# Kernel optimization log

Hardware: AMD Instinct MI355X
Metric: run time of the kernel (lower is better)

The kernel has to match this reference:

```python
import jax, jax.numpy as jnp
import numpy as np

N = 50000        # nodes
E = 1600000      # edges (before self-loops)
HID = 128
HEADS = 4
HD = HID // HEADS
FIN = 32 + 7     # node feats + scenario feats
EPS = 1e-5


def _ln(x, g, b):
    m = x.mean(-1, keepdims=True)
    v = ((x - m) ** 2).mean(-1, keepdims=True)
    return (x - m) / jnp.sqrt(v + EPS) * g + b


def _gat(x, src, dst, W, a_s, a_d, bias):
    # PyG GATConv (concat=True, negative_slope=0.2), eval mode (no dropout)
    xp = (x @ W).reshape(-1, HEADS, HD)                    # [N,H,C]
    es = (xp * a_s).sum(-1)                                # [N,H]
    ed = (xp * a_d).sum(-1)                                # [N,H]
    e = jax.nn.leaky_relu(es[src] + ed[dst], 0.2)          # [Etot,H]
    emax = jax.ops.segment_max(e, dst, num_segments=N)     # per-target softmax (self-loops guarantee nonempty segments)
    a = jnp.exp(e - emax[dst])
    denom = jax.ops.segment_sum(a, dst, num_segments=N)
    a = a / denom[dst]
    out = jax.ops.segment_sum(xp[src] * a[:, :, None], dst, num_segments=N)
    return out.reshape(-1, HID) + bias


def setup_inputs() -> dict:
    key = jax.random.key(0)
    ks = iter(jax.random.split(key, 64))

    def rn(shape, scale=0.05):
        return jax.random.normal(next(ks), shape, dtype=jnp.float32) * scale

    inp = {}
    inp["x"] = jax.random.normal(next(ks), (N, FIN), dtype=jnp.float32)
    inp["edge_index"] = jax.random.randint(next(ks), (2, E), 0, N)
    inp["enc_w1"] = rn((FIN, HID)); inp["enc_b1"] = jnp.zeros((HID,), jnp.float32)
    inp["enc_w2"] = rn((HID, HID)); inp["enc_b2"] = jnp.zeros((HID,), jnp.float32)
    for l in (1, 2, 3):
        inp[f"W{l}"] = rn((HID, HID))
        inp[f"as{l}"] = rn((HEADS, HD))
        inp[f"ad{l}"] = rn((HEADS, HD))
        inp[f"bc{l}"] = jnp.zeros((HID,), jnp.float32)
        inp[f"g{l}"] = jnp.ones((HID,), jnp.float32)
        inp[f"be{l}"] = jnp.zeros((HID,), jnp.float32)
    inp["imp_w1"] = rn((HID, HID // 2)); inp["imp_b1"] = jnp.zeros((HID // 2,), jnp.float32)
    inp["imp_w2"] = rn((HID // 2, 3));   inp["imp_b2"] = jnp.zeros((3,), jnp.float32)
    inp["tim_w1"] = rn((HID, HID // 2)); inp["tim_b1"] = jnp.zeros((HID // 2,), jnp.float32)
    inp["tim_w2"] = rn((HID // 2, 2));   inp["tim_b2"] = jnp.zeros((2,), jnp.float32)
    return inp


def reference(x, edge_index, enc_w1, enc_b1, enc_w2, enc_b2,
              W1, as1, ad1, bc1, g1, be1,
              W2, as2, ad2, bc2, g2, be2,
              W3, as3, ad3, bc3, g3, be3,
              imp_w1, imp_b1, imp_w2, imp_b2,
              tim_w1, tim_b1, tim_w2, tim_b2):
    loops = jnp.arange(N, dtype=edge_index.dtype)          # add_self_loops=True
    src = jnp.concatenate([edge_index[0], loops])
    dst = jnp.concatenate([edge_index[1], loops])
    h = jax.nn.relu(x @ enc_w1 + enc_b1) @ enc_w2 + enc_b2
    for (W, a_s, a_d, bc, g, be) in ((W1, as1, ad1, bc1, g1, be1),
                                     (W2, as2, ad2, bc2, g2, be2),
                                     (W3, as3, ad3, bc3, g3, be3)):
        h = jax.nn.relu(_ln(_gat(h, src, dst, W, a_s, a_d, bc) + h, g, be))
    impact = jax.nn.relu(h @ imp_w1 + imp_b1) @ imp_w2 + imp_b2
    timing = jax.nn.softplus(jax.nn.relu(h @ tim_w1 + tim_b1) @ tim_w2 + tim_b2)
    return (impact, timing)
```

## Files before the change

kernel.cpp:

```cpp
#include <hip/hip_runtime.h>
#include <hip/hip_bf16.h>
#include <math.h>

#define NN 50000
#define EDGES 1600000
#define ETOT (EDGES + NN)
#define FINDIM 39
#define NPART 128
#define PSZ 391
#define PCAP 14000
#define P1TILE 4096

__device__ __forceinline__ unsigned pack_bf16(float a, float b) {
    __hip_bfloat162 t;
    t.x = __float2bfloat16(a);
    t.y = __float2bfloat16(b);
    return *(unsigned*)&t;
}
__device__ __forceinline__ float2 unpack_bf16(unsigned w) {
    float2 r;
    r.x = __uint_as_float(w << 16);
    r.y = __uint_as_float(w & 0xffff0000u);
    return r;
}

__device__ __forceinline__ int src_at(const int* ei, int i, bool i32) {
    return i32 ? ei[i] : ei[2 * i];
}
__device__ __forceinline__ int dst_at(const int* ei, int i, bool i32) {
    return i32 ? ei[EDGES + i] : ei[2 * (EDGES + i)];
}

__global__ __launch_bounds__(256) void pass1_kernel(const int* __restrict__ ei,
                                                    int* __restrict__ gcursor,
                                                    unsigned* __restrict__ pbuf) {
    __shared__ unsigned raw[P1TILE];
    __shared__ unsigned srt[P1TILE];
    __shared__ int pcnt[NPART], poff[NPART], pcur[NPART], gb[NPART];
    __shared__ int i32flag;
    int t = threadIdx.x;
    if (t == 0) i32flag = 0;
    __syncthreads();
    int chunk = (ETOT + gridDim.x - 1) / gridDim.x;
    int c0 = blockIdx.x * chunk;
    int c1 = c0 + chunk; if (c1 > ETOT) c1 = ETOT;
    int sb = c0 < EDGES - 64 ? c0 : 0;
    if (t < 64 && ei[2 * (sb + t) + 1] != 0) i32flag = 1;
    __syncthreads();
    bool i32 = (i32flag != 0);
    for (int t0 = c0; t0 < c1; t0 += P1TILE) {
        int tn = c1 - t0; if (tn > P1TILE) tn = P1TILE;
        if (t < NPART) { pcnt[t] = 0; pcur[t] = 0; }
        __syncthreads();
        for (int i = t; i < tn; i += 256) {
            int e = t0 + i;
            int s, d;
            if (e < EDGES) { s = src_at(ei, e, i32); d = dst_at(ei, e, i32); }
            else { s = d = e - EDGES; }
            raw[i] = ((unsigned)s << 16) | (unsigned)d;
            atomicAdd(&pcnt[d / PSZ], 1);
        }
        __syncthreads();
        if (t < NPART) poff[t] = pcnt[t];
        __syncthreads();
        for (int off = 1; off < NPART; off <<= 1) {
            int v = 0;
            if (t < NPART && t >= off) v = poff[t - off];
            __syncthreads();
            if (t < NPART) poff[t] += v;
            __syncthreads();
        }
        if (t < NPART) {
            poff[t] -= pcnt[t];
            gb[t] = atomicAdd(&gcursor[t], pcnt[t]);
        }
        __syncthreads();
        for (int i = t; i < tn; i += 256) {
            unsigned r = raw[i];
            int part = (int)(r & 0xFFFFu) / PSZ;
            int pos = poff[part] + atomicAdd(&pcur[part], 1);
            srt[pos] = r;
        }
        __syncthreads();
        for (int i = t; i < tn; i += 256) {
            unsigned r = srt[i];
            int part = (int)(r & 0xFFFFu) / PSZ;
            int gpos = gb[part] + (i - poff[part]);
            if (gpos < PCAP) pbuf[(size_t)part * PCAP + gpos] = r;
        }
        __syncthreads();
    }
}

__global__ __launch_bounds__(128) void scan_part_kernel(const int* __restrict__ gcursor,
                                                        int* __restrict__ pbase,
                                                        int* __restrict__ rowptrN) {
    __shared__ int sm[NPART];
    int t = threadIdx.x;
    int v = gcursor[t];
    sm[t] = v;
    __syncthreads();
    for (int off = 1; off < NPART; off <<= 1) {
        int x = (t >= off) ? sm[t - off] : 0;
        __syncthreads();
        sm[t] += x;
        __syncthreads();
    }
    pbase[t] = sm[t] - v;
    if (t == NPART - 1) *rowptrN = sm[t];
}

__global__ __launch_bounds__(256) void pass2_kernel(const unsigned* __restrict__ pbuf,
                                                    const int* __restrict__ gcursor,
                                                    const int* __restrict__ pbase,
                                                    int* __restrict__ rowptr,
                                                    int* __restrict__ colidx) {
    __shared__ unsigned recs[PCAP];
    __shared__ int lhist[PSZ], lexcl[PSZ], lcur[PSZ];
    int p = blockIdx.x;
    int t = threadIdx.x;
    int n = gcursor[p]; if (n > PCAP) n = PCAP;
    int base = pbase[p];
    int d0 = p * PSZ;
    int nd = NN - d0; if (nd > PSZ) nd = PSZ;
    for (int i = t; i < nd; i += 256) { lhist[i] = 0; lcur[i] = 0; }
    __syncthreads();
    for (int i = t; i < n; i += 256) {
        unsigned r = pbuf[(size_t)p * PCAP + i];
        recs[i] = r;
        atomicAdd(&lhist[(int)(r & 0xFFFFu) - d0], 1);
    }
    __syncthreads();
    for (int i = t; i < nd; i += 256) lexcl[i] = lhist[i];
    __syncthreads();
    for (int off = 1; off < PSZ; off <<= 1) {
        int a0 = 0, a1 = 0;
        int i0 = t, i1 = t + 256;
        if (i0 < nd && i0 >= off) a0 = lexcl[i0 - off];
        if (i1 < nd && i1 >= off) a1 = lexcl[i1 - off];
        __syncthreads();
        if (i0 < nd) lexcl[i0] += a0;
        if (i1 < nd) lexcl[i1] += a1;
        __syncthreads();
    }
    for (int i = t; i < nd; i += 256) {
        lexcl[i] -= lhist[i];
        rowptr[d0 + i] = base + lexcl[i];
    }
    __syncthreads();
    for (int i = t; i < n; i += 256) {
        unsigned r = recs[i];
        int li = (int)(r & 0xFFFFu) - d0;
        int pos = base + lexcl[li] + atomicAdd(&lcur[li], 1);
        colidx[pos] = (int)(r >> 16);
    }
}

template <int NC, bool RELU>
__global__ __launch_bounds__(256) void gemm_small_kernel(const float* __restrict__ A,
                                                         const float* __restrict__ B,
                                                         const float* __restrict__ bias,
                                                         float* __restrict__ C, int M, int K) {
    constexpr int TM = 32;
    constexpr int GROUPS = 256 / NC;
    constexpr int RPG = TM / GROUPS;
    constexpr int KC = 64;
    __shared__ float As[TM * 128];
    __shared__ float Bs[KC * NC];
    int t = threadIdx.x;
    int i0 = blockIdx.x * TM;

    int rows = M - i0; if (rows > TM) rows = TM;
    for (int idx = t; idx < rows * K; idx += 256) {
        int r = idx / K, k = idx - r * K;
        As[r * K + k] = A[(size_t)(i0 + r) * K + k];
    }

    int col = t % NC, grp = t / NC;
    int rg0 = grp * RPG;
    float acc[RPG];
#pragma unroll
    for (int r = 0; r < RPG; ++r) acc[r] = 0.f;

    for (int k0 = 0; k0 < K; k0 += KC) {
        int kc = K - k0; if (kc > KC) kc = KC;
        __syncthreads();
        for (int idx = t; idx < kc * NC; idx += 256) Bs[idx] = B[(size_t)k0 * NC + idx];
        __syncthreads();
        for (int k = 0; k < kc; ++k) {
            float bv = Bs[k * NC + col];
#pragma unroll
            for (int r = 0; r < RPG; ++r) acc[r] += As[(rg0 + r) * K + k0 + k] * bv;
        }
    }

    float bb = bias ? bias[col] : 0.f;
#pragma unroll
    for (int r = 0; r < RPG; ++r) {
        int i = i0 + rg0 + r;
        if (i < M) {
            float v = acc[r] + bb;
            if (RELU) v = v > 0.f ? v : 0.f;
            C[(size_t)i * NC + col] = v;
        }
    }
}

template <bool BIAS, bool EPI>
__global__ __launch_bounds__(256) void gemm128_kernel(const float* __restrict__ A,
                                                      const float* __restrict__ B,
                                                      const float* __restrict__ bias,
                                                      float* __restrict__ C,
                                                      unsigned* __restrict__ XP,
                                                      const float* __restrict__ a_s,
                                                      const float* __restrict__ a_d,
                                                      float* __restrict__ es,
                                                      float* __restrict__ ed, int M) {
    __shared__ float As[64 * 32];
    __shared__ float Bs[32 * 128];
    int t = threadIdx.x;
    int i0 = blockIdx.x * 64;
    int tc = t & 31;
    int tr = t >> 5;
    int r0 = tr * 8;
    int c0 = tc * 4;

    float acc[8][4];
#pragma unroll
    for (int i = 0; i < 8; ++i)
#pragma unroll
        for (int j = 0; j < 4; ++j) acc[i][j] = 0.f;

    for (int k0 = 0; k0 < 128; k0 += 32) {
        __syncthreads();
#pragma unroll
        for (int q = 0; q < 2; ++q) {
            int idx = t + q * 256;
            int r = idx >> 3, kq = idx & 7;
            float4 v4 = make_float4(0.f, 0.f, 0.f, 0.f);
            if (i0 + r < M) v4 = *(const float4*)&A[(size_t)(i0 + r) * 128 + k0 + kq * 4];
            *(float4*)&As[r * 32 + kq * 4] = v4;
        }
#pragma unroll
        for (int q = 0; q < 4; ++q) {
            int idx = (t + q * 256) * 4;
            *(float4*)&Bs[idx] = *(const float4*)&B[(size_t)k0 * 128 + idx];
        }
        __syncthreads();
#pragma unroll 8
        for (int k = 0; k < 32; k += 4) {
            float4 a4[8];
#pragma unroll
            for (int i = 0; i < 8; ++i)
                a4[i] = *(const float4*)&As[(r0 + i) * 32 + k];
            float4 b4[4];
#pragma unroll
            for (int kk = 0; kk < 4; ++kk)
                b4[kk] = *(const float4*)&Bs[(k + kk) * 128 + c0];
#pragma unroll
            for (int i = 0; i < 8; ++i) {
                const float* av = (const float*)&a4[i];
#pragma unroll
                for (int kk = 0; kk < 4; ++kk) {
                    acc[i][0] += av[kk] * b4[kk].x;
                    acc[i][1] += av[kk] * b4[kk].y;
                    acc[i][2] += av[kk] * b4[kk].z;
                    acc[i][3] += av[kk] * b4[kk].w;
                }
            }
        }
    }

    if (!EPI) {
        float4 bias4 = make_float4(0.f, 0.f, 0.f, 0.f);
        if (BIAS) bias4 = *(const float4*)&bias[c0];
#pragma unroll
        for (int i = 0; i < 8; ++i) {
            int row = i0 + r0 + i;
            if (row < M) {
                float4 o;
                o.x = acc[i][0] + bias4.x;
                o.y = acc[i][1] + bias4.y;
                o.z = acc[i][2] + bias4.z;
                o.w = acc[i][3] + bias4.w;
                *(float4*)&C[(size_t)row * 128 + c0] = o;
            }
        }
    } else {
#pragma unroll
        for (int i = 0; i < 8; ++i) {
            int row = i0 + r0 + i;
            if (row < M) {
                uint2 o;
                o.x = pack_bf16(acc[i][0], acc[i][1]);
                o.y = pack_bf16(acc[i][2], acc[i][3]);
                *(uint2*)&XP[(size_t)row * 64 + tc * 2] = o;
            }
        }
        int hd = tc >> 3;
        float4 s4 = *(const float4*)&a_s[c0];
        float4 d4 = *(const float4*)&a_d[c0];
#pragma unroll
        for (int i = 0; i < 8; ++i) {
            int row = i0 + r0 + i;
            float s = acc[i][0] * s4.x + acc[i][1] * s4.y + acc[i][2] * s4.z + acc[i][3] * s4.w;
            float d = acc[i][0] * d4.x + acc[i][1] * d4.y + acc[i][2] * d4.z + acc[i][3] * d4.w;
#pragma unroll
            for (int off = 4; off >= 1; off >>= 1) {
                s += __shfl_xor(s, off);
                d += __shfl_xor(d, off);
            }
            if ((tc & 7) == 0 && row < M) {
                es[row * 4 + hd] = s;
                ed[row * 4 + hd] = d;
            }
        }
    }
}

__global__ __launch_bounds__(256) void gemm_heads_kernel(const float* __restrict__ A,
                                                         const float* __restrict__ iw1,
                                                         const float* __restrict__ ib1,
                                                         const float* __restrict__ tw1,
                                                         const float* __restrict__ tb1,
                                                         const float* __restrict__ iw2,
                                                         const float* __restrict__ ib2,
                                                         const float* __restrict__ tw2,
                                                         const float* __restrict__ tb2,
                                                         float* __restrict__ out, int M) {
    __shared__ float As[64 * 32];
    __shared__ float Bs[32 * 128];
    int t = threadIdx.x;
    int i0 = blockIdx.x * 64;
    int tc = t & 31;
    int tr = t >> 5;
    int r0 = tr * 8;
    int c0 = tc * 4;

    float acc[8][4];
#pragma unroll
    for (int i = 0; i < 8; ++i)
#pragma unroll
        for (int j = 0; j < 4; ++j) acc[i][j] = 0.f;

    for (int k0 = 0; k0 < 128; k0 += 32) {
        __syncthreads();
#pragma unroll
        for (int q = 0; q < 2; ++q) {
            int idx = t + q * 256;
            int r = idx >> 3, kq = idx & 7;
            float4 v4 = make_float4(0.f, 0.f, 0.f, 0.f);
            if (i0 + r < M) v4 = *(const float4*)&A[(size_t)(i0 + r) * 128 + k0 + kq * 4];
            *(float4*)&As[r * 32 + kq * 4] = v4;
        }
#pragma unroll
        for (int q = 0; q < 4; ++q) {
            int idx = (t + q * 256) * 4;
            int k = idx >> 7, cl = idx & 127;
            float4 v4 = (cl < 64)
                ? *(const float4*)&iw1[(size_t)(k0 + k) * 64 + cl]
                : *(const float4*)&tw1[(size_t)(k0 + k) * 64 + (cl - 64)];
            *(float4*)&Bs[idx] = v4;
        }
        __syncthreads();
#pragma unroll 8
        for (int k = 0; k < 32; k += 4) {
            float4 a4[8];
#pragma unroll
            for (int i = 0; i < 8; ++i)
                a4[i] = *(const float4*)&As[(r0 + i) * 32 + k];
            float4 b4[4];
#pragma unroll
            for (int kk = 0; kk < 4; ++kk)
                b4[kk] = *(const float4*)&Bs[(k + kk) * 128 + c0];
#pragma unroll
            for (int i = 0; i < 8; ++i) {
                const float* av = (const float*)&a4[i];
#pragma unroll
                for (int kk = 0; kk < 4; ++kk) {
                    acc[i][0] += av[kk] * b4[kk].x;
                    acc[i][1] += av[kk] * b4[kk].y;
                    acc[i][2] += av[kk] * b4[kk].z;
                    acc[i][3] += av[kk] * b4[kk].w;
                }
            }
        }
    }

    bool isimp = (tc < 16);
    int lc = isimp ? c0 : (c0 - 64);
    float v[8][4];
#pragma unroll
    for (int i = 0; i < 8; ++i)
#pragma unroll
        for (int j = 0; j < 4; ++j) {
            float b = isimp ? ib1[lc + j] : tb1[lc + j];
            float x = acc[i][j] + b;
            v[i][j] = x > 0.f ? x : 0.f;
        }
#pragma unroll
    for (int i = 0; i < 8; ++i) {
        int row = i0 + r0 + i;
        if (isimp) {
#pragma unroll
            for (int c = 0; c < 3; ++c) {
                float pc = v[i][0] * iw2[(lc + 0) * 3 + c] + v[i][1] * iw2[(lc + 1) * 3 + c]
                         + v[i][2] * iw2[(lc + 2) * 3 + c] + v[i][3] * iw2[(lc + 3) * 3 + c];
#pragma unroll
                for (int off = 8; off >= 1; off >>= 1) pc += __shfl_xor(pc, off);
                if (tc == 0 && row < M) out[(size_t)row * 3 + c] = pc + ib2[c];
            }
        } else {
#pragma unroll
            for (int d = 0; d < 2; ++d) {
                float pd = v[i][0] * tw2[(lc + 0) * 2 + d] + v[i][1] * tw2[(lc + 1) * 2 + d]
                         + v[i][2] * tw2[(lc + 2) * 2 + d] + v[i][3] * tw2[(lc + 3) * 2 + d];
#pragma unroll
                for (int off = 8; off >= 1; off >>= 1) pd += __shfl_xor(pd, off);
                if (tc == 16 && row < M) {
                    float a = pd + tb2[d];
                    float sp = a > 20.f ? a : log1pf(__expf(a));
                    out[(size_t)(NN * 3) + (size_t)row * 2 + d] = sp;
                }
            }
        }
    }
}

__global__ __launch_bounds__(256) void gat_kernel(const unsigned* __restrict__ xpk,
                                                  const float* __restrict__ es,
                                                  const float* __restrict__ ed,
                                                  const int* __restrict__ rowptr,
                                                  const int* __restrict__ colidx,
                                                  float* __restrict__ h,
                                                  const float* __restrict__ bc,
                                                  const float* __restrict__ g,
                                                  const float* __restrict__ be) {
    int wv = threadIdx.x >> 6, l = threadIdx.x & 63;
    int v = blockIdx.x * 4 + wv;
    if (v >= NN) return;
    int s0 = rowptr[v], s1 = rowptr[v + 1];
    int hd = l >> 4;
    float edv = ed[v * 4 + hd];
    float ax = 0.f, ay = 0.f, den = 0.f;
    int p = s0;
    for (; p + 8 <= s1; p += 8) {
        int u[8];
#pragma unroll
        for (int q = 0; q < 8; ++q) u[q] = colidx[p + q];
        unsigned xw[8];
#pragma unroll
        for (int q = 0; q < 8; ++q) xw[q] = xpk[(size_t)u[q] * 64 + l];
        float w[8];
#pragma unroll
        for (int q = 0; q < 8; ++q) {
            float e = es[u[q] * 4 + hd] + edv;
            e = e > 0.f ? e : 0.2f * e;
            w[q] = __expf(e);
        }
#pragma unroll
        for (int q = 0; q < 8; ++q) {
            float2 x = unpack_bf16(xw[q]);
            ax += w[q] * x.x; ay += w[q] * x.y; den += w[q];
        }
    }
    for (; p < s1; ++p) {
        int u = colidx[p];
        float e = es[u * 4 + hd] + edv; e = e > 0.f ? e : 0.2f * e;
        float w = __expf(e);
        float2 x = unpack_bf16(xpk[(size_t)u * 64 + l]);
        ax += w * x.x; ay += w * x.y;
        den += w;
    }
    float rd = 1.f / den;

    float2 h2  = *(const float2*)&h[(size_t)v * 128 + 2 * l];
    float2 bc2 = *(const float2*)&bc[2 * l];
    float y0 = ax * rd + bc2.x + h2.x;
    float y1 = ay * rd + bc2.y + h2.y;

    float s = y0 + y1;
#pragma unroll
    for (int off = 32; off >= 1; off >>= 1) s += __shfl_xor(s, off);
    float mean = s * (1.f / 128.f);
    float d0 = y0 - mean, d1 = y1 - mean;
    float vv = d0 * d0 + d1 * d1;
#pragma unroll
    for (int off = 32; off >= 1; off >>= 1) vv += __shfl_xor(vv, off);
    float rstd = rsqrtf(vv * (1.f / 128.f) + 1e-5f);
    float2 g2  = *(const float2*)&g[2 * l];
    float2 be2 = *(const float2*)&be[2 * l];
    float z0 = d0 * rstd * g2.x + be2.x;
    float z1 = d1 * rstd * g2.y + be2.y;
    float2 o;
    o.x = z0 > 0.f ? z0 : 0.f;
    o.y = z1 > 0.f ? z1 : 0.f;
    *(float2*)&h[(size_t)v * 128 + 2 * l] = o;
}

extern "C" void kernel_launch(void* const* d_in, const int* in_sizes, int n_in,
                              void* d_out, int out_size, void* d_ws, size_t ws_size,
                              hipStream_t stream) {
    const float* x      = (const float*)d_in[0];
    const int*   ei     = (const int*)d_in[1];
    const float* enc_w1 = (const float*)d_in[2];
    const float* enc_b1 = (const float*)d_in[3];
    const float* enc_w2 = (const float*)d_in[4];
    const float* enc_b2 = (const float*)d_in[5];
    const float *W[3], *as_[3], *ad_[3], *bc[3], *g[3], *be[3];
    for (int l = 0; l < 3; ++l) {
        W[l]   = (const float*)d_in[6 + l * 6 + 0];
        as_[l] = (const float*)d_in[6 + l * 6 + 1];
        ad_[l] = (const float*)d_in[6 + l * 6 + 2];
        bc[l]  = (const float*)d_in[6 + l * 6 + 3];
        g[l]   = (const float*)d_in[6 + l * 6 + 4];
        be[l]  = (const float*)d_in[6 + l * 6 + 5];
    }
    const float* imp_w1 = (const float*)d_in[24];
    const float* imp_b1 = (const float*)d_in[25];
    const float* imp_w2 = (const float*)d_in[26];
    const float* imp_b2 = (const float*)d_in[27];
    const float* tim_w1 = (const float*)d_in[28];
    const float* tim_b1 = (const float*)d_in[29];
    const float* tim_w2 = (const float*)d_in[30];
    const float* tim_b2 = (const float*)d_in[31];

    int* gcursor = (int*)d_ws;
    int* pbase   = gcursor + NPART;
    int* rowptr  = pbase + NPART + 64;
    int* colidx  = rowptr + NN + 1;
    uintptr_t pb = (uintptr_t)(colidx + ETOT);
    pb = (pb + 255) & ~(uintptr_t)255;
    unsigned* pbuf = (unsigned*)pb;
    uintptr_t fb = (uintptr_t)(pbuf + (size_t)NPART * PCAP);
    fb = (fb + 255) & ~(uintptr_t)255;
    float* es = (float*)fb;
    float* ed = es + (size_t)NN * 4;
    float* h  = ed + (size_t)NN * 4;
    float* xpf = h + (size_t)NN * 128;
    unsigned* xpk = (unsigned*)xpf;
    float* tmp = xpf;

    hipMemsetAsync(gcursor, 0, NPART * sizeof(int), stream);
    pass1_kernel<<<512, 256, 0, stream>>>(ei, gcursor, pbuf);
    scan_part_kernel<<<1, NPART, 0, stream>>>(gcursor, pbase, rowptr + NN);
    pass2_kernel<<<NPART, 256, 0, stream>>>(pbuf, gcursor, pbase, rowptr, colidx);

    const int GB64 = (NN + 63) / 64;
    gemm_small_kernel<128, true><<<(NN + 31) / 32, 256, 0, stream>>>(x, enc_w1, enc_b1, tmp, NN, FINDIM);
    gemm128_kernel<true, false><<<GB64, 256, 0, stream>>>(tmp, enc_w2, enc_b2, h, nullptr,
                                                          nullptr, nullptr, nullptr, nullptr, NN);

    for (int l = 0; l < 3; ++l) {
        gemm128_kernel<false, true><<<GB64, 256, 0, stream>>>(h, W[l], nullptr, nullptr, xpk,
                                                              as_[l], ad_[l], es, ed, NN);
        gat_kernel<<<(NN + 3) / 4, 256, 0, stream>>>(xpk, es, ed, rowptr, colidx, h,
                                                     bc[l], g[l], be[l]);
    }

    gemm_heads_kernel<<<GB64, 256, 0, stream>>>(h, imp_w1, imp_b1, tim_w1, tim_b1,
                                                imp_w2, imp_b2, tim_w2, tim_b2,
                                                (float*)d_out, NN);
}
```

Baseline: 589.7 us.

## Compute edge weights cooperatively across lanes and broadcast via bpermute; fold partition scan into pass2

The GAT aggregation now has 16 edges x 4 heads spread across the 64 lanes. Each lane loads one colidx/es entry and computes one exp, and the results are broadcast to the lanes that need them with ds_bpermute. Before, every lane redundantly computed exp for every edge of its head. Separately, the tiny partition-scan kernel is removed and each pass2 block recomputes the 128-entry scan in shared memory, saving one launch. The tradeoff is extra bpermute traffic in the inner loop and redundant scan work in every pass2 block.

After: 713.2 us. 20.9% more time.

```diff
diff --git a/kernel.cpp b/kernel.cpp
--- a/kernel.cpp
+++ b/kernel.cpp
@@ -92,35 +92,27 @@
     }
 }
 
-__global__ __launch_bounds__(128) void scan_part_kernel(const int* __restrict__ gcursor,
-                                                        int* __restrict__ pbase,
-                                                        int* __restrict__ rowptrN) {
-    __shared__ int sm[NPART];
-    int t = threadIdx.x;
-    int v = gcursor[t];
-    sm[t] = v;
-    __syncthreads();
-    for (int off = 1; off < NPART; off <<= 1) {
-        int x = (t >= off) ? sm[t - off] : 0;
-        __syncthreads();
-        sm[t] += x;
-        __syncthreads();
-    }
-    pbase[t] = sm[t] - v;
-    if (t == NPART - 1) *rowptrN = sm[t];
-}
-
 __global__ __launch_bounds__(256) void pass2_kernel(const unsigned* __restrict__ pbuf,
                                                     const int* __restrict__ gcursor,
-                                                    const int* __restrict__ pbase,
                                                     int* __restrict__ rowptr,
                                                     int* __restrict__ colidx) {
     __shared__ unsigned recs[PCAP];
     __shared__ int lhist[PSZ], lexcl[PSZ], lcur[PSZ];
+    __shared__ int psm[NPART];
     int p = blockIdx.x;
     int t = threadIdx.x;
+    if (t < NPART) psm[t] = gcursor[t];
+    __syncthreads();
+    for (int off = 1; off < NPART; off <<= 1) {
+        int x = 0;
+        if (t < NPART && t >= off) x = psm[t - off];
+        __syncthreads();
+        if (t < NPART) psm[t] += x;
+        __syncthreads();
+    }
     int n = gcursor[p]; if (n > PCAP) n = PCAP;
-    int base = pbase[p];
+    int base = psm[p] - gcursor[p];
+    if (p == NPART - 1 && t == 0) rowptr[NN] = psm[NPART - 1];
     int d0 = p * PSZ;
     int nd = NN - d0; if (nd > PSZ) nd = PSZ;
     for (int i = t; i < nd; i += 256) { lhist[i] = 0; lcur[i] = 0; }
@@ -441,36 +433,33 @@
     if (v >= NN) return;
     int s0 = rowptr[v], s1 = rowptr[v + 1];
     int hd = l >> 4;
-    float edv = ed[v * 4 + hd];
+    int q4 = l & 3;
+    int e  = l >> 2;
+    float edq = ed[v * 4 + q4];
     float ax = 0.f, ay = 0.f, den = 0.f;
-    int p = s0;
-    for (; p + 8 <= s1; p += 8) {
-        int u[8];
-#pragma unroll
-        for (int q = 0; q < 8; ++q) u[q] = colidx[p + q];
-        unsigned xw[8];
-#pragma unroll
-        for (int q = 0; q < 8; ++q) xw[q] = xpk[(size_t)u[q] * 64 + l];
-        float w[8];
-#pragma unroll
-        for (int q = 0; q < 8; ++q) {
-            float e = es[u[q] * 4 + hd] + edv;
-            e = e > 0.f ? e : 0.2f * e;
-            w[q] = __expf(e);
-        }
-#pragma unroll
-        for (int q = 0; q < 8; ++q) {
-            float2 x = unpack_bf16(xw[q]);
-            ax += w[q] * x.x; ay += w[q] * x.y; den += w[q];
-        }
-    }
-    for (; p < s1; ++p) {
-        int u = colidx[p];
-        float e = es[u * 4 + hd] + edv; e = e > 0.f ? e : 0.2f * e;
-        float w = __expf(e);
-        float2 x = unpack_bf16(xpk[(size_t)u * 64 + l]);
-        ax += w * x.x; ay += w * x.y;
-        den += w;
+
+    for (int p = s0; p < s1; p += 16) {
+        int n = s1 - p; if (n > 16) n = 16;
+        int ureg = 0;
+        float wreg = 0.f;
+        if (e < n) {
+            ureg = colidx[p + e];
+            float tt = es[(unsigned)((ureg << 2) + q4)] + edq;
+            tt = tt > 0.f ? tt : 0.2f * tt;
+            wreg = __expf(tt);
+        }
+        int wbits = __float_as_int(wreg);
+        int bidx = hd << 2;
+#pragma unroll 4
+        for (int q = 0; q < n; ++q) {
+            int u = __builtin_amdgcn_ds_bpermute(bidx, ureg);
+            float w = __int_as_float(__builtin_amdgcn_ds_bpermute(bidx, wbits));
+            bidx += 16;
+            float2 x = unpack_bf16(xpk[(unsigned)((u << 6) + l)]);
+            ax = fmaf(w, x.x, ax);
+            ay = fmaf(w, x.y, ay);
+            den += w;
+        }
     }
     float rd = 1.f / den;
 
@@ -526,8 +515,7 @@
     const float* tim_b2 = (const float*)d_in[31];
 
     int* gcursor = (int*)d_ws;
-    int* pbase   = gcursor + NPART;
-    int* rowptr  = pbase + NPART + 64;
+    int* rowptr  = gcursor + NPART + 64;
     int* colidx  = rowptr + NN + 1;
     uintptr_t pb = (uintptr_t)(colidx + ETOT);
     pb = (pb + 255) & ~(uintptr_t)255;
@@ -543,8 +531,7 @@
 
     hipMemsetAsync(gcursor, 0, NPART * sizeof(int), stream);
     pass1_kernel<<<512, 256, 0, stream>>>(ei, gcursor, pbuf);
-    scan_part_kernel<<<1, NPART, 0, stream>>>(gcursor, pbase, rowptr + NN);
-    pass2_kernel<<<NPART, 256, 0, stream>>>(pbuf, gcursor, pbase, rowptr, colidx);
+    pass2_kernel<<<NPART, 256, 0, stream>>>(pbuf, gcursor, rowptr, colidx);
 
     const int GB64 = (NN + 63) / 64;
     gemm_small_kernel<128, true><<<(NN + 31) / 32, 256, 0, stream>>>(x, enc_w1, enc_b1, tmp, NN, FINDIM);
```

## Double CSR partitions, fold partition scan into pass2, tighten GAT indexing

Applied to the files above, without the earlier changes.

Doubles the number of destination partitions to 256 with smaller partitions, which gives pass2 twice as many blocks and uses less shared memory per block. The standalone partition-scan kernel is removed, and each pass2 block now recomputes the 256-entry prefix sum itself, saving one launch. The GAT aggregation switches to 32-bit index arithmetic, fmax-based leaky ReLU and explicit FMAs to trim instruction count. The redundant per-block scan adds a little work, and the smaller PCAP of 7100 leaves less headroom against partition overflow (about 6450 expected per partition).

Result: faster. 570.4 us (-3.3%).

```diff
diff --git a/kernel.cpp b/kernel.cpp
--- a/kernel.cpp
+++ b/kernel.cpp
@@ -6,9 +6,9 @@
 #define EDGES 1600000
 #define ETOT (EDGES + NN)
 #define FINDIM 39
-#define NPART 128
-#define PSZ 391
-#define PCAP 14000
+#define NPART 256
+#define PSZ 196
+#define PCAP 7100
 #define P1TILE 4096
 
 __device__ __forceinline__ unsigned pack_bf16(float a, float b) {
@@ -50,7 +50,7 @@
     bool i32 = (i32flag != 0);
     for (int t0 = c0; t0 < c1; t0 += P1TILE) {
         int tn = c1 - t0; if (tn > P1TILE) tn = P1TILE;
-        if (t < NPART) { pcnt[t] = 0; pcur[t] = 0; }
+        pcnt[t] = 0; pcur[t] = 0;
         __syncthreads();
         for (int i = t; i < tn; i += 256) {
             int e = t0 + i;
@@ -61,19 +61,16 @@
             atomicAdd(&pcnt[d / PSZ], 1);
         }
         __syncthreads();
-        if (t < NPART) poff[t] = pcnt[t];
+        poff[t] = pcnt[t];
         __syncthreads();
         for (int off = 1; off < NPART; off <<= 1) {
-            int v = 0;
-            if (t < NPART && t >= off) v = poff[t - off];
+            int v = (t >= off) ? poff[t - off] : 0;
             __syncthreads();
-            if (t < NPART) poff[t] += v;
+            poff[t] += v;
             __syncthreads();
         }
-        if (t < NPART) {
-            poff[t] -= pcnt[t];
-            gb[t] = atomicAdd(&gcursor[t], pcnt[t]);
-        }
+        poff[t] -= pcnt[t];
+        gb[t] = atomicAdd(&gcursor[t], pcnt[t]);
         __syncthreads();
         for (int i = t; i < tn; i += 256) {
             unsigned r = raw[i];
@@ -92,37 +89,29 @@
     }
 }
 
-__global__ __launch_bounds__(128) void scan_part_kernel(const int* __restrict__ gcursor,
-                                                        int* __restrict__ pbase,
-                                                        int* __restrict__ rowptrN) {
-    __shared__ int sm[NPART];
-    int t = threadIdx.x;
-    int v = gcursor[t];
-    sm[t] = v;
-    __syncthreads();
-    for (int off = 1; off < NPART; off <<= 1) {
-        int x = (t >= off) ? sm[t - off] : 0;
-        __syncthreads();
-        sm[t] += x;
-        __syncthreads();
-    }
-    pbase[t] = sm[t] - v;
-    if (t == NPART - 1) *rowptrN = sm[t];
-}
-
 __global__ __launch_bounds__(256) void pass2_kernel(const unsigned* __restrict__ pbuf,
                                                     const int* __restrict__ gcursor,
-                                                    const int* __restrict__ pbase,
                                                     int* __restrict__ rowptr,
                                                     int* __restrict__ colidx) {
     __shared__ unsigned recs[PCAP];
     __shared__ int lhist[PSZ], lexcl[PSZ], lcur[PSZ];
+    __shared__ int psm[NPART];
     int p = blockIdx.x;
     int t = threadIdx.x;
+    psm[t] = gcursor[t];
+    __syncthreads();
+    for (int off = 1; off < NPART; off <<= 1) {
+        int x = (t >= off) ? psm[t - off] : 0;
+        __syncthreads();
+        psm[t] += x;
+        __syncthreads();
+    }
     int n = gcursor[p]; if (n > PCAP) n = PCAP;
-    int base = pbase[p];
+    int base = psm[p] - gcursor[p];
+    if (p == NPART - 1 && t == 0) rowptr[NN] = psm[NPART - 1];
     int d0 = p * PSZ;
     int nd = NN - d0; if (nd > PSZ) nd = PSZ;
+    if (nd < 0) nd = 0;
     for (int i = t; i < nd; i += 256) { lhist[i] = 0; lcur[i] = 0; }
     __syncthreads();
     for (int i = t; i < n; i += 256) {
@@ -134,13 +123,10 @@
     for (int i = t; i < nd; i += 256) lexcl[i] = lhist[i];
     __syncthreads();
     for (int off = 1; off < PSZ; off <<= 1) {
-        int a0 = 0, a1 = 0;
-        int i0 = t, i1 = t + 256;
-        if (i0 < nd && i0 >= off) a0 = lexcl[i0 - off];
-        if (i1 < nd && i1 >= off) a1 = lexcl[i1 - off];
-        __syncthreads();
-        if (i0 < nd) lexcl[i0] += a0;
-        if (i1 < nd) lexcl[i1] += a1;
+        int a0 = 0;
+        if (t < nd && t >= off) a0 = lexcl[t - off];
+        __syncthreads();
+        if (t < nd) lexcl[t] += a0;
         __syncthreads();
     }
     for (int i = t; i < nd; i += 256) {
@@ -441,7 +427,7 @@
     if (v >= NN) return;
     int s0 = rowptr[v], s1 = rowptr[v + 1];
     int hd = l >> 4;
-    float edv = ed[v * 4 + hd];
+    float edv = ed[(unsigned)(v << 2) + hd];
     float ax = 0.f, ay = 0.f, den = 0.f;
     int p = s0;
     for (; p + 8 <= s1; p += 8) {
@@ -450,26 +436,30 @@
         for (int q = 0; q < 8; ++q) u[q] = colidx[p + q];
         unsigned xw[8];
 #pragma unroll
-        for (int q = 0; q < 8; ++q) xw[q] = xpk[(size_t)u[q] * 64 + l];
+        for (int q = 0; q < 8; ++q) xw[q] = xpk[(unsigned)(u[q] << 6) + l];
         float w[8];
 #pragma unroll
         for (int q = 0; q < 8; ++q) {
-            float e = es[u[q] * 4 + hd] + edv;
-            e = e > 0.f ? e : 0.2f * e;
+            float e = es[(unsigned)(u[q] << 2) + hd] + edv;
+            e = fmaxf(e, 0.2f * e);
             w[q] = __expf(e);
         }
 #pragma unroll
         for (int q = 0; q < 8; ++q) {
             float2 x = unpack_bf16(xw[q]);
-            ax += w[q] * x.x; ay += w[q] * x.y; den += w[q];
+            ax = fmaf(w[q], x.x, ax);
+            ay = fmaf(w[q], x.y, ay);
+            den += w[q];
         }
     }
     for (; p < s1; ++p) {
         int u = colidx[p];
-        float e = es[u * 4 + hd] + edv; e = e > 0.f ? e : 0.2f * e;
+        float e = es[(unsigned)(u << 2) + hd] + edv;
+        e = fmaxf(e, 0.2f * e);
         float w = __expf(e);
-        float2 x = unpack_bf16(xpk[(size_t)u * 64 + l]);
-        ax += w * x.x; ay += w * x.y;
+        float2 x = unpack_bf16(xpk[(unsigned)(u << 6) + l]);
+        ax = fmaf(w, x.x, ax);
+        ay = fmaf(w, x.y, ay);
         den += w;
     }
     float rd = 1.f / den;
@@ -526,8 +516,7 @@
     const float* tim_b2 = (const float*)d_in[31];
 
     int* gcursor = (int*)d_ws;
-    int* pbase   = gcursor + NPART;
-    int* rowptr  = pbase + NPART + 64;
+    int* rowptr  = gcursor + NPART + 64;
     int* colidx  = rowptr + NN + 1;
     uintptr_t pb = (uintptr_t)(colidx + ETOT);
     pb = (pb + 255) & ~(uintptr_t)255;
@@ -543,8 +532,7 @@
 
     hipMemsetAsync(gcursor, 0, NPART * sizeof(int), stream);
     pass1_kernel<<<512, 256, 0, stream>>>(ei, gcursor, pbuf);
-    scan_part_kernel<<<1, NPART, 0, stream>>>(gcursor, pbase, rowptr + NN);
-    pass2_kernel<<<NPART, 256, 0, stream>>>(pbuf, gcursor, pbase, rowptr, colidx);
+    pass2_kernel<<<NPART, 256, 0, stream>>>(pbuf, gcursor, rowptr, colidx);
 
     const int GB64 = (NN + 63) / 64;
     gemm_small_kernel<128, true><<<(NN + 31) / 32, 256, 0, stream>>>(x, enc_w1, enc_b1, tmp, NN, FINDIM);
```
